# Kernel tuning notes

Hardware: AMD Instinct MI355X
Metric: run time of the kernel (lower is better)

The kernel has to match this reference:

```python
import jax, jax.numpy as jnp
import numpy as np

N, E, G, NH, H = 50000, 400000, 1024, 64, 1
EPS = 1e-5

def _bn(x):
    # BatchNorm1d in training mode, affine at init (gamma=1, beta=0), biased var
    m = x.mean(0)
    v = ((x - m) ** 2).mean(0)
    return (x - m) * jax.lax.rsqrt(v + EPS)

def _seg_softmax(logits, seg, num_segments):
    # numerically stable per-segment softmax (torch_geometric.utils.softmax)
    mx = jax.ops.segment_max(logits, seg, num_segments=num_segments)
    e = jnp.exp(logits - mx[seg])
    s = jax.ops.segment_sum(e, seg, num_segments=num_segments)
    return e / s[seg]

def setup_inputs() -> dict:
    key = jax.random.key(0)
    ks = jax.random.split(key, 16)
    p = lambda k, shape, s=0.1: jax.random.normal(k, shape, jnp.float32) * s
    return {
        "x": jax.random.normal(ks[0], (N, 92), jnp.float32),
        "edge_index": jax.random.randint(ks[1], (2, E), 0, N),
        "edge_attr": jax.random.normal(ks[2], (E, 41), jnp.float32),
        "batch": jnp.sort(jax.random.randint(ks[3], (N,), 0, G)),
        "global_feat": jax.random.normal(ks[4], (G, 103), jnp.float32),
        "emb_n_W": p(ks[5], (92, NH)), "emb_n_b": jnp.zeros((NH,), jnp.float32),
        "emb_e_W": p(ks[6], (41, NH)), "emb_e_b": jnp.zeros((NH,), jnp.float32),
        "conv_W": p(ks[7], (3, 2 * NH, H * NH)),
        "conv_att": p(ks[8], (3, H, 2 * NH)),
        "conv_bias": jnp.zeros((3, H * NH), jnp.float32),
        "comp_node_W": p(ks[9], (NH + 103, 32)), "comp_node_b": jnp.zeros((32,), jnp.float32),
        "comp_att_W": p(ks[10], (32, 1)), "comp_att_b": jnp.zeros((1,), jnp.float32),
        "fc_W": p(ks[11], (NH, 1)), "fc_b": jnp.zeros((1,), jnp.float32),
    }

def reference(x, edge_index, edge_attr, batch, global_feat,
              emb_n_W, emb_n_b, emb_e_W, emb_e_b,
              conv_W, conv_att, conv_bias,
              comp_node_W, comp_node_b, comp_att_W, comp_att_b,
              fc_W, fc_b):
    sp = jax.nn.softplus
    src, dst = edge_index[0], edge_index[1]  # PyG: x_j = x[src], aggregate by dst
    h = x @ emb_n_W + emb_n_b                              # [N, NH]
    ea = jax.nn.leaky_relu(edge_attr @ emb_e_W + emb_e_b, 0.2)  # [E, NH]
    for l in range(3):  # AGATConv layers
        hi = jnp.concatenate([h[dst], ea], -1)             # [E, 2*NH]
        hj = jnp.concatenate([h[src], ea], -1)
        ti = sp(hi @ conv_W[l]).reshape(E, H, NH)
        tj = sp(hj @ conv_W[l]).reshape(E, H, NH)
        alpha = sp(jnp.sum(jnp.concatenate([ti, tj], -1) * conv_att[l][None], -1))  # [E, H]
        alpha = sp(_bn(alpha))
        alpha = _seg_softmax(alpha, dst, N)                # segment softmax per dst node
        agg = jax.ops.segment_sum(tj * alpha[..., None], dst, num_segments=N)  # [N, H, NH]
        h = agg.reshape(N, H * NH) + conv_bias[l]
        h = sp(_bn(h))                                     # outer BatchNorm1d + softplus
    # composition attention: repeat_interleave(global_feat, counts) == gather by graph id
    gf = global_feat[batch]                                # [N, 103]
    a = sp(jnp.concatenate([h, gf], -1) @ comp_node_W + comp_node_b) @ comp_att_W + comp_att_b
    w = _seg_softmax(a, batch, G)                          # [N, 1]
    pooled = jax.ops.segment_sum(h * w, batch, num_segments=G)  # global_add_pool
    return pooled @ fc_W + fc_b                            # [G, 1]
```

## Files before the change

### kernel.cpp

```cpp
#include <hip/hip_runtime.h>
#include <hip/hip_bf16.h>
#include <hip/hip_fp16.h>
#include <math.h>


typedef unsigned short ushortt;
typedef _Float16 half2v __attribute__((ext_vector_type(2)));
typedef _Float16 f16x8 __attribute__((ext_vector_type(8)));
typedef float f32x4 __attribute__((ext_vector_type(4)));

__device__ __forceinline__ float sp_f(float x) {
  return x > 20.0f ? x : __logf(1.0f + __expf(x));
}
__device__ __forceinline__ float h2f(ushortt u) {
  union { ushortt u; __half h; } c; c.u = u;
  return __half2float(c.h);
}
__device__ __forceinline__ ushortt f2h(float f) {
  union { __half h; ushortt u; } c; c.h = __float2half(f);
  return c.u;
}
__device__ __forceinline__ float4 h4_to_f4(ushort4 u) {
  return make_float4(h2f(u.x), h2f(u.y), h2f(u.z), h2f(u.w));
}
__device__ __forceinline__ unsigned pack2h(float a, float b) {
  union { _Float16 h[2]; unsigned u; } c;
  c.h[0] = (_Float16)a; c.h[1] = (_Float16)b;
  return c.u;
}

#define SLOTS 2304

template<int K, int ACT, int BIAS, int GATHER, int FUSE_BN,
         typename IT, typename OT>
__global__ __launch_bounds__(256) void k_gemm_rt(
    const IT* __restrict__ in, const float* __restrict__ W,
    const float* __restrict__ b, OT* __restrict__ out, int R,
    const int* __restrict__ rows, const float* __restrict__ csbn, float invN)
{
  constexpr int KP = (K + 3) / 4 * 4;
  constexpr int LS = KP + 4;
  __shared__ __align__(16) float ins[64 * LS];
  __shared__ __align__(16) float Ws[KP * 64];
  __shared__ float bnm[64], bns[64];

  const int tx = threadIdx.x;
  const int b0 = blockIdx.x * 64;

  if (FUSE_BN) {
    if (tx < 64) {
      float mn = 0.f, sq = 0.f;
      #pragma unroll
      for (int bk = 0; bk < 16; ++bk) {
        mn += csbn[bk * 128 + tx];
        sq += csbn[bk * 128 + 64 + tx];
      }
      mn *= invN; sq *= invN;
      bnm[tx] = mn;
      bns[tx] = rsqrtf(sq - mn * mn + 1e-5f);
    }
    __syncthreads();
  }

  for (int i = tx; i < KP * 64; i += 256) {
    const int k = i >> 6;
    Ws[i] = (k < K) ? W[i] : 0.0f;
  }
  for (int i = tx; i < 64 * (KP / 4); i += 256) {
    const int row = i / (KP / 4);
    const int k4 = i % (KP / 4);
    long r = b0 + row; if (r >= R) r = R - 1;
    if (GATHER) r = rows[r];
    float4 v;
    if (K % 4 == 0) {
      v = *(const float4*)&((const float*)in)[r * (long)K + k4 * 4];
    } else {
      float t[4];
      #pragma unroll
      for (int j = 0; j < 4; ++j) {
        const int k = k4 * 4 + j;
        t[j] = (k < K) ? ((const float*)in)[r * (long)K + k] : 0.0f;
      }
      v = make_float4(t[0], t[1], t[2], t[3]);
    }
    if (FUSE_BN) {
      float* vv = (float*)&v;
      #pragma unroll
      for (int j = 0; j < 4; ++j) {
        const int c = k4 * 4 + j;
        vv[j] = sp_f((vv[j] - bnm[c]) * bns[c]);
      }
    }
    *(float4*)&ins[row * LS + k4 * 4] = v;
  }
  __syncthreads();

  const int lr0 = ((tx >> 6) << 4) + (((tx >> 4) & 3) << 2);
  const int c0 = (tx & 15) << 2;
  float acc[4][4];
  #pragma unroll
  for (int i = 0; i < 4; ++i)
    #pragma unroll
    for (int j = 0; j < 4; ++j) acc[i][j] = 0.0f;

  #pragma unroll 4
  for (int k4 = 0; k4 < KP / 4; ++k4) {
    float4 w[4], a[4];
    #pragma unroll
    for (int kk = 0; kk < 4; ++kk)
      w[kk] = *(const float4*)&Ws[(k4 * 4 + kk) * 64 + c0];
    #pragma unroll
    for (int ri = 0; ri < 4; ++ri)
      a[ri] = *(const float4*)&ins[(lr0 + ri) * LS + k4 * 4];
    #pragma unroll
    for (int ri = 0; ri < 4; ++ri) {
      const float* av = (const float*)&a[ri];
      #pragma unroll
      for (int kk = 0; kk < 4; ++kk) {
        acc[ri][0] = fmaf(av[kk], w[kk].x, acc[ri][0]);
        acc[ri][1] = fmaf(av[kk], w[kk].y, acc[ri][1]);
        acc[ri][2] = fmaf(av[kk], w[kk].z, acc[ri][2]);
        acc[ri][3] = fmaf(av[kk], w[kk].w, acc[ri][3]);
      }
    }
  }

  float4 bias = make_float4(0.f, 0.f, 0.f, 0.f);
  if (BIAS) bias = *(const float4*)&b[c0];
  #pragma unroll
  for (int ri = 0; ri < 4; ++ri) {
    const long r = b0 + lr0 + ri;
    if (r >= R) continue;
    float4 v;
    v.x = acc[ri][0] + bias.x; v.y = acc[ri][1] + bias.y;
    v.z = acc[ri][2] + bias.z; v.w = acc[ri][3] + bias.w;
    if (ACT == 1) {
      v.x = v.x >= 0.f ? v.x : 0.2f * v.x;  v.y = v.y >= 0.f ? v.y : 0.2f * v.y;
      v.z = v.z >= 0.f ? v.z : 0.2f * v.z;  v.w = v.w >= 0.f ? v.w : 0.2f * v.w;
    }
    if (sizeof(OT) == 4) {
      *(float4*)&out[r * 64 + c0] = v;
    } else {
      ushort4 u;
      u.x = f2h(v.x); u.y = f2h(v.y); u.z = f2h(v.z); u.w = f2h(v.w);
      *(ushort4*)&out[r * 64 + c0] = u;
    }
  }
}

__global__ __launch_bounds__(512) void k_packW(
    const float* __restrict__ convW, uint4* __restrict__ WBg)
{
  const int l3 = blockIdx.x;
  const float* W = convW + (size_t)l3 * 128 * 64 + 64 * 64;
  const int idx = threadIdx.x;
  const int kstep = idx >> 8;
  const int rem = idx & 255;
  const int ncol = rem >> 6;
  const int l = rem & 63;
  const int kbase = kstep * 32 + (l >> 4) * 8;
  const int n = ncol * 16 + (l & 15);
  ushortt tmp[8];
  #pragma unroll
  for (int j = 0; j < 8; ++j) tmp[j] = f2h(W[(kbase + j) * 64 + n]);
  WBg[l3 * 512 + idx] = *(uint4*)tmp;
}

__global__ __launch_bounds__(256) void k_efused(
    const ushortt* __restrict__ ea, const uint4* __restrict__ WBg,
    ushortt* __restrict__ out, int E, const ushortt* __restrict__ P,
    const int* __restrict__ srcp, const int* __restrict__ dstp,
    const float* __restrict__ catt, float* __restrict__ a1,
    float* __restrict__ stats)
{
  __shared__ __align__(16) unsigned char smem[17408];
  __shared__ float atts[128];
  __shared__ float ssum[4], ssq[4];
  ushortt* As   = (ushortt*)smem;
  uint4*   WB   = (uint4*)(smem + 9216);
  float*   accs = (float*)smem;

  const int tx = threadIdx.x;
  const int b0 = blockIdx.x * 64;
  const int lane = tx & 63;
  const int w = tx >> 6;

  if (tx < 128) atts[tx] = catt[tx];
  #pragma unroll
  for (int i = tx; i < 64 * 8; i += 256) {
    const int row = i >> 3;
    const int k8 = i & 7;
    long r = b0 + row; if (r >= E) r = E - 1;
    *(uint4*)&As[row * 72 + k8 * 8] = *(const uint4*)&ea[r * (long)64 + k8 * 8];
  }
  #pragma unroll
  for (int i = tx; i < 512; i += 256) WB[i] = WBg[i];
  __syncthreads();

  const int lr0 = ((tx >> 6) << 4) + (((tx >> 4) & 3) << 2);
  const int c0 = (tx & 15) << 2;
  ushort4 pdv[4], psv[4];
  #pragma unroll
  for (int ri = 0; ri < 4; ++ri) {
    long e = b0 + lr0 + ri; if (e >= E) e = E - 1;
    const int s = srcp[e];
    const int d = dstp[e];
    psv[ri] = *(const ushort4*)&P[(long)s * 64 + c0];
    pdv[ri] = *(const ushort4*)&P[(long)d * 64 + c0];
  }

  f32x4 acc0 = {0.f,0.f,0.f,0.f}, acc1 = {0.f,0.f,0.f,0.f};
  f32x4 acc2 = {0.f,0.f,0.f,0.f}, acc3 = {0.f,0.f,0.f,0.f};
  const int arow = 16 * w + (lane & 15);
  #pragma unroll
  for (int kstep = 0; kstep < 2; ++kstep) {
    const f16x8 a = __builtin_bit_cast(f16x8,
        *(const uint4*)&As[arow * 72 + kstep * 32 + (lane >> 4) * 8]);
    const int bb = kstep * 256 + lane;
    const f16x8 b0v = __builtin_bit_cast(f16x8, WB[bb]);
    const f16x8 b1v = __builtin_bit_cast(f16x8, WB[bb + 64]);
    const f16x8 b2v = __builtin_bit_cast(f16x8, WB[bb + 128]);
    const f16x8 b3v = __builtin_bit_cast(f16x8, WB[bb + 192]);
    acc0 = __builtin_amdgcn_mfma_f32_16x16x32_f16(a, b0v, acc0, 0, 0, 0);
    acc1 = __builtin_amdgcn_mfma_f32_16x16x32_f16(a, b1v, acc1, 0, 0, 0);
    acc2 = __builtin_amdgcn_mfma_f32_16x16x32_f16(a, b2v, acc2, 0, 0, 0);
    acc3 = __builtin_amdgcn_mfma_f32_16x16x32_f16(a, b3v, acc3, 0, 0, 0);
  }
  __syncthreads();

  {
    const int rbase = 16 * w + (lane >> 4) * 4;
    const int cb = lane & 15;
    #pragma unroll
    for (int reg = 0; reg < 4; ++reg) {
      accs[(rbase + reg) * 68 + cb]      = acc0[reg];
      accs[(rbase + reg) * 68 + 16 + cb] = acc1[reg];
      accs[(rbase + reg) * 68 + 32 + cb] = acc2[reg];
      accs[(rbase + reg) * 68 + 48 + cb] = acc3[reg];
    }
  }
  __syncthreads();

  float s1 = 0.f, s2 = 0.f;
  #pragma unroll
  for (int ri = 0; ri < 4; ++ri) {
    const long e = b0 + lr0 + ri;
    float part = 0.0f;
    if (e < E) {
      const float4 Pd = h4_to_f4(pdv[ri]);
      const float4 Ps = h4_to_f4(psv[ri]);
      const float4 m = *(const float4*)&accs[(lr0 + ri) * 68 + c0];
      float tj[4];
      const float ti0 = sp_f(Pd.x + m.x);
      const float ti1 = sp_f(Pd.y + m.y);
      const float ti2 = sp_f(Pd.z + m.z);
      const float ti3 = sp_f(Pd.w + m.w);
      tj[0] = sp_f(Ps.x + m.x);
      tj[1] = sp_f(Ps.y + m.y);
      tj[2] = sp_f(Ps.z + m.z);
      tj[3] = sp_f(Ps.w + m.w);
      ushort4 u;
      u.x = f2h(tj[0]); u.y = f2h(tj[1]); u.z = f2h(tj[2]); u.w = f2h(tj[3]);
      *(ushort4*)&out[e * 64 + c0] = u;
      part = ti0 * atts[c0] + ti1 * atts[c0 + 1] + ti2 * atts[c0 + 2] + ti3 * atts[c0 + 3]
           + tj[0] * atts[64 + c0] + tj[1] * atts[64 + c0 + 1]
           + tj[2] * atts[64 + c0 + 2] + tj[3] * atts[64 + c0 + 3];
    }
    #pragma unroll
    for (int off = 8; off; off >>= 1) part += __shfl_xor(part, off);
    if ((tx & 15) == 0 && e < E) {
      const float v = sp_f(part);
      a1[e] = v;
      s1 += v; s2 += v * v;
    }
  }
  s1 += __shfl_xor(s1, 16); s2 += __shfl_xor(s2, 16);
  s1 += __shfl_xor(s1, 32); s2 += __shfl_xor(s2, 32);
  if ((tx & 63) == 0) { ssum[tx >> 6] = s1; ssq[tx >> 6] = s2; }
  __syncthreads();
  if (tx == 0) {
    const int bk = blockIdx.x & 63;
    atomicAdd(&stats[bk], ssum[0] + ssum[1] + ssum[2] + ssum[3]);
    atomicAdd(&stats[64 + bk], ssq[0] + ssq[1] + ssq[2] + ssq[3]);
  }
}

__global__ __launch_bounds__(256) void k_count(
    const int* __restrict__ dst, int* __restrict__ counts, int E)
{
  for (int i = blockIdx.x * 256 + threadIdx.x; i < E; i += gridDim.x * 256)
    atomicAdd(&counts[dst[i]], 1);
}

__global__ __launch_bounds__(256) void k_scan1(
    const int* __restrict__ counts, int* __restrict__ offs,
    int* __restrict__ bsum, int N)
{
  __shared__ int sm[256];
  const int t = threadIdx.x;
  const int idx = blockIdx.x * 256 + t;
  const int v = (idx < N) ? counts[idx] : 0;
  sm[t] = v;
  __syncthreads();
  for (int off = 1; off < 256; off <<= 1) {
    const int u = (t >= off) ? sm[t - off] : 0;
    __syncthreads();
    sm[t] += u;
    __syncthreads();
  }
  if (idx < N) offs[idx] = sm[t] - v;
  if (t == 255) bsum[blockIdx.x] = sm[255];
}

__global__ __launch_bounds__(1024) void k_scan2(int* __restrict__ bsum, int SB)
{
  __shared__ int sm[1024];
  const int t = threadIdx.x;
  const int v = (t < SB) ? bsum[t] : 0;
  sm[t] = v;
  __syncthreads();
  for (int off = 1; off < 1024; off <<= 1) {
    const int u = (t >= off) ? sm[t - off] : 0;
    __syncthreads();
    sm[t] += u;
    __syncthreads();
  }
  if (t < SB) bsum[t] = sm[t] - v;
}

__global__ __launch_bounds__(256) void k_scan3(
    int* __restrict__ offs, const int* __restrict__ bsum, int N, int E)
{
  const int idx = blockIdx.x * 256 + threadIdx.x;
  if (idx < N) offs[idx] += bsum[blockIdx.x];
  if (idx == 0) offs[N] = E;
}

__global__ __launch_bounds__(256) void k_fill(
    const int* __restrict__ dst, const int* __restrict__ offs,
    int* __restrict__ cursors, int* __restrict__ eids, int E)
{
  for (int i = blockIdx.x * 256 + threadIdx.x; i < E; i += gridDim.x * 256) {
    const int d = dst[i];
    eids[offs[d] + atomicAdd(&cursors[d], 1)] = i;
  }
}

__global__ __launch_bounds__(256) void k_permidx(
    const int* __restrict__ eids, const int* __restrict__ eidx,
    int* __restrict__ srcp, int* __restrict__ dstp, int E)
{
  for (int i = blockIdx.x * 256 + threadIdx.x; i < E; i += gridDim.x * 256) {
    const int e = eids[i];
    srcp[i] = eidx[e];
    dstp[i] = eidx[(long)E + e];
  }
}

__global__ __launch_bounds__(256) void k_aggregate(
    const int* __restrict__ offs, const float* __restrict__ a1p,
    const ushortt* __restrict__ Mp, const float* __restrict__ stats,
    float invE, float* __restrict__ aggn, float* __restrict__ cs, int N)
{
  __shared__ float sm_mean, sm_scl;
  const int tx = threadIdx.x;
  if (tx < 64) {
    float s1 = stats[tx];
    float s2 = stats[64 + tx];
    #pragma unroll
    for (int off = 32; off; off >>= 1) {
      s1 += __shfl_xor(s1, off);
      s2 += __shfl_xor(s2, off);
    }
    if (tx == 0) {
      const float mean = s1 * invE;
      sm_mean = mean;
      sm_scl = rsqrtf(s2 * invE - mean * mean + 1e-5f);
    }
  }
  __syncthreads();
  const float mean = sm_mean;
  const float scl = sm_scl;

  const int t = tx & 63;
  const int wid = tx >> 6;
  float s = 0.f, s2 = 0.f;
  const long step = (long)gridDim.x * 4;
  for (long n = (long)blockIdx.x * 4 + wid; n < N; n += step) {
    const int o0 = offs[n];
    const int o1 = offs[n + 1];
    float av = 0.f, sew = 0.f;
    #pragma unroll 4
    for (int i = o0; i < o1; ++i) {
      const float w = __expf(sp_f((a1p[i] - mean) * scl));
      av = fmaf(h2f(Mp[(long)i * 64 + t]), w, av);
      sew += w;
    }
    const float v = (o1 > o0) ? av / sew : 0.0f;
    aggn[n * 64 + t] = v;
    s += v; s2 += v * v;
  }
  __shared__ float b1[256], b2[256];
  b1[tx] = s; b2[tx] = s2;
  __syncthreads();
  if (tx < 64) {
    const int bank = (blockIdx.x & 15) * 128;
    atomicAdd(&cs[bank + t], b1[t] + b1[64 + t] + b1[128 + t] + b1[192 + t]);
    atomicAdd(&cs[bank + 64 + t], b2[t] + b2[64 + t] + b2[128 + t] + b2[192 + t]);
  }
}

__global__ __launch_bounds__(256) void k_hnew(
    const float* __restrict__ aggn, const float* __restrict__ cs,
    float invN, float* __restrict__ h, int N)
{
  const int c = threadIdx.x & 63;
  const int r = threadIdx.x >> 6;
  float mn = 0.f, sq = 0.f;
  #pragma unroll
  for (int bk = 0; bk < 16; ++bk) {
    mn += cs[bk * 128 + c];
    sq += cs[bk * 128 + 64 + c];
  }
  mn *= invN; sq *= invN;
  const float scl = rsqrtf(sq - mn * mn + 1e-5f);
  for (long n = (long)blockIdx.x * 4 + r; n < N; n += (long)gridDim.x * 4)
    h[n * 64 + c] = sp_f((aggn[n * 64 + c] - mn) * scl);
}

#define QSS 170
__global__ __launch_bounds__(256) void k_comp(
    const float* __restrict__ h, const float* __restrict__ gf,
    const int* __restrict__ batch, const float* __restrict__ Wc,
    const float* __restrict__ bc, const float* __restrict__ aw,
    const float* __restrict__ ab, float* __restrict__ aN, int N)
{
  __shared__ __align__(16) float qs[64 * QSS];
  __shared__ __align__(16) float Wcs[167 * 32];
  __shared__ float aws[32], bcs[32];
  const int tx = threadIdx.x;
  const int b0 = blockIdx.x * 64;
  for (int i = tx; i < 167 * 32; i += 256) Wcs[i] = Wc[i];
  if (tx < 32) { aws[tx] = aw[tx]; bcs[tx] = bc[tx]; }
  for (int i = tx; i < 64 * 16; i += 256) {
    const int n = i >> 4;
    const int c4 = (i & 15) << 2;
    long r = b0 + n; if (r >= N) r = N - 1;
    *(float4*)&qs[n * QSS + c4] = *(const float4*)&h[r * 64 + c4];
  }
  for (int i = tx; i < 64 * 103; i += 256) {
    const int n = i / 103;
    const int c = i % 103;
    long r = b0 + n; if (r >= N) r = N - 1;
    qs[n * QSS + 64 + c] = gf[(long)batch[r] * 103 + c];
  }
  __syncthreads();

  const int n = tx >> 2;
  const int colg = (tx & 3) << 3;
  float acc[8];
  #pragma unroll
  for (int j = 0; j < 8; ++j) acc[j] = 0.f;
  #pragma unroll 2
  for (int k = 0; k < 167; ++k) {
    const float q = qs[n * QSS + k];
    const float4 w0 = *(const float4*)&Wcs[k * 32 + colg];
    const float4 w1 = *(const float4*)&Wcs[k * 32 + colg + 4];
    acc[0] = fmaf(q, w0.x, acc[0]);
    acc[1] = fmaf(q, w0.y, acc[1]);
    acc[2] = fmaf(q, w0.z, acc[2]);
    acc[3] = fmaf(q, w0.w, acc[3]);
    acc[4] = fmaf(q, w1.x, acc[4]);
    acc[5] = fmaf(q, w1.y, acc[5]);
    acc[6] = fmaf(q, w1.z, acc[6]);
    acc[7] = fmaf(q, w1.w, acc[7]);
  }
  float val = 0.f;
  #pragma unroll
  for (int j = 0; j < 8; ++j)
    val += sp_f(acc[j] + bcs[colg + j]) * aws[colg + j];
  val += __shfl_xor(val, 1);
  val += __shfl_xor(val, 2);
  const long r = b0 + n;
  if ((tx & 3) == 0 && r < N) aN[r] = val + ab[0];
}

__global__ __launch_bounds__(64) void k_pool(
    const float* __restrict__ h, const float* __restrict__ aN,
    const int* __restrict__ batch, const float* __restrict__ fcW,
    const float* __restrict__ fcb, float* __restrict__ out, int N, int G)
{
  const int g = blockIdx.x;
  const int t = threadIdx.x;
  int lo = 0, hi = N;
  while (lo < hi) { int mid = (lo + hi) >> 1; if (batch[mid] < g) lo = mid + 1; else hi = mid; }
  const int s = lo;
  hi = N;
  while (lo < hi) { int mid = (lo + hi) >> 1; if (batch[mid] < g + 1) lo = mid + 1; else hi = mid; }
  const int e2 = lo;
  if (s >= e2) { if (t == 0) out[g] = fcb[0]; return; }
  float mx = -1e30f;
  for (int i = s + t; i < e2; i += 64) mx = fmaxf(mx, aN[i]);
  #pragma unroll
  for (int off = 32; off; off >>= 1) mx = fmaxf(mx, __shfl_xor(mx, off));
  float se = 0.f;
  for (int i = s + t; i < e2; i += 64) se += __expf(aN[i] - mx);
  #pragma unroll
  for (int off = 32; off; off >>= 1) se += __shfl_xor(se, off);
  float acc = 0.f;
  for (int n = s; n < e2; ++n) {
    const float w = __expf(aN[n] - mx);
    acc = fmaf(h[(long)n * 64 + t], w, acc);
  }
  float part = (acc / se) * fcW[t];
  #pragma unroll
  for (int off = 32; off; off >>= 1) part += __shfl_xor(part, off);
  if (t == 0) out[g] = part + fcb[0];
}

extern "C" void kernel_launch(void* const* d_in, const int* in_sizes, int n_in,
                              void* d_out, int out_size, void* d_ws, size_t ws_size,
                              hipStream_t stream)
{
  const float* x     = (const float*)d_in[0];
  const int*   eidx  = (const int*)  d_in[1];
  const float* eattr = (const float*)d_in[2];
  const int*   batch = (const int*)  d_in[3];
  const float* gfeat = (const float*)d_in[4];
  const float* embnW = (const float*)d_in[5];
  const float* embnb = (const float*)d_in[6];
  const float* embeW = (const float*)d_in[7];
  const float* embeb = (const float*)d_in[8];
  const float* convW = (const float*)d_in[9];
  const float* convA = (const float*)d_in[10];
  const float* compW = (const float*)d_in[12];
  const float* compb = (const float*)d_in[13];
  const float* attW  = (const float*)d_in[14];
  const float* attb  = (const float*)d_in[15];
  const float* fcW   = (const float*)d_in[16];
  const float* fcb   = (const float*)d_in[17];
  float* out = (float*)d_out;

  const int N = in_sizes[0] / 92;
  const int E = in_sizes[1] / 2;
  const int G = in_sizes[4] / 103;
  const float invN = 1.0f / (float)N;
  const float invE = 1.0f / (float)E;

  char* pw = (char*)d_ws;
  float* h     = (float*)pw;  pw += (size_t)N * 64 * 4;
  float* aggn  = (float*)pw;  pw += (size_t)N * 64 * 4;
  float* aE    = (float*)pw;  pw += (size_t)E * 4;
  float* statsB = (float*)pw; pw += 3 * SLOTS * 4;
  float* aN    = (float*)pw;  pw += (size_t)N * 4;
  int* counts  = (int*)pw;    pw += (size_t)N * 4;
  int* cursors = (int*)pw;    pw += (size_t)N * 4;
  int* offs    = (int*)pw;    pw += ((size_t)N + 1) * 4;
  int* bsum    = (int*)pw;    pw += 1024 * 4;
  int* eids    = (int*)pw;    pw += (size_t)E * 4;
  int* srcp    = (int*)pw;    pw += (size_t)E * 4;
  int* dstp    = (int*)pw;    pw += (size_t)E * 4;
  pw = (char*)(((size_t)pw + 63) & ~(size_t)63);
  uint4* WBg   = (uint4*)pw;   pw += 3 * 512 * 16;
  ushortt* Pp  = (ushortt*)pw; pw += (size_t)N * 64 * 2;
  ushortt* ea  = (ushortt*)pw; pw += (size_t)E * 64 * 2;
  ushortt* M   = (ushortt*)pw;

  const int gE64 = (E + 63) / 64;
  const int gN64 = (N + 63) / 64;
  const int SB = (N + 255) / 256;

  hipMemsetAsync(counts, 0, 2 * (size_t)N * sizeof(int), stream);
  hipMemsetAsync(statsB, 0, 3 * SLOTS * sizeof(float), stream);
  k_count<<<2048, 256, 0, stream>>>(eidx + E, counts, E);
  k_scan1<<<SB, 256, 0, stream>>>(counts, offs, bsum, N);
  k_scan2<<<1, 1024, 0, stream>>>(bsum, SB);
  k_scan3<<<SB, 256, 0, stream>>>(offs, bsum, N, E);
  k_fill<<<2048, 256, 0, stream>>>(eidx + E, offs, cursors, eids, E);
  k_permidx<<<2048, 256, 0, stream>>>(eids, eidx, srcp, dstp, E);
  k_packW<<<3, 512, 0, stream>>>(convW, WBg);

  k_gemm_rt<92, 0, 1, 0, 0, float, float><<<gN64, 256, 0, stream>>>(
      x, embnW, embnb, h, N, nullptr, nullptr, 0.f);
  k_gemm_rt<41, 1, 1, 1, 0, float, ushortt><<<gE64, 256, 0, stream>>>(
      eattr, embeW, embeb, ea, E, eids, nullptr, 0.f);

  for (int l = 0; l < 3; ++l) {
    const float* Wl = convW + (size_t)l * 128 * 64;
    const float* Al = convA + (size_t)l * 128;
    float* statsL = statsB + (size_t)l * SLOTS;
    if (l == 0) {
      k_gemm_rt<64, 0, 0, 0, 0, float, ushortt><<<gN64, 256, 0, stream>>>(
          h, Wl, nullptr, Pp, N, nullptr, nullptr, 0.f);
    } else {
      k_gemm_rt<64, 0, 0, 0, 1, float, ushortt><<<gN64, 256, 0, stream>>>(
          aggn, Wl, nullptr, Pp, N, nullptr,
          statsB + (size_t)(l - 1) * SLOTS + 128, invN);
    }
    k_efused<<<gE64, 256, 0, stream>>>(ea, WBg + (size_t)l * 512, M, E,
                                       Pp, srcp, dstp, Al, aE, statsL);
    k_aggregate<<<2048, 256, 0, stream>>>(offs, aE, M, statsL,
                                          invE, aggn, statsL + 128, N);
  }

  k_hnew<<<2048, 256, 0, stream>>>(aggn, statsB + 2 * SLOTS + 128, invN, h, N);
  k_comp<<<gN64, 256, 0, stream>>>(h, gfeat, batch, compW, compb, attW, attb, aN, N);
  k_pool<<<G, 64, 0, stream>>>(h, aN, batch, fcW, fcb, out, N, G);

  (void)n_in; (void)out_size; (void)ws_size;
}
```

Before: 475.6 us.

## Embed edges in original order then permute fp16 rows; fuse index permutation into fill

The edge-embedding GEMM no longer gathers its 41-float input rows by sorted edge id. It writes fp16 output in original order to a temp buffer, and a new kernel permutes the 128-byte rows into dst-sorted order. The fill kernel now writes srcp/dstp directly, which removes the separate permidx pass. The shared-memory row stride is also padded to avoid bank conflicts. The cost is an extra E×128B buffer plus a read/write pass in exchange for coalesced GEMM input loads.

```diff
diff --git a/kernel.cpp b/kernel.cpp
--- a/kernel.cpp
+++ b/kernel.cpp
@@ -5,7 +5,6 @@
 
 
 typedef unsigned short ushortt;
-typedef _Float16 half2v __attribute__((ext_vector_type(2)));
 typedef _Float16 f16x8 __attribute__((ext_vector_type(8)));
 typedef float f32x4 __attribute__((ext_vector_type(4)));
 
@@ -23,23 +22,18 @@
 __device__ __forceinline__ float4 h4_to_f4(ushort4 u) {
   return make_float4(h2f(u.x), h2f(u.y), h2f(u.z), h2f(u.w));
 }
-__device__ __forceinline__ unsigned pack2h(float a, float b) {
-  union { _Float16 h[2]; unsigned u; } c;
-  c.h[0] = (_Float16)a; c.h[1] = (_Float16)b;
-  return c.u;
-}
 
 #define SLOTS 2304
 
-template<int K, int ACT, int BIAS, int GATHER, int FUSE_BN,
-         typename IT, typename OT>
+template<int K, int ACT, int BIAS, int FUSE_BN, typename IT, typename OT>
 __global__ __launch_bounds__(256) void k_gemm_rt(
     const IT* __restrict__ in, const float* __restrict__ W,
     const float* __restrict__ b, OT* __restrict__ out, int R,
-    const int* __restrict__ rows, const float* __restrict__ csbn, float invN)
+    const float* __restrict__ csbn, float invN)
 {
   constexpr int KP = (K + 3) / 4 * 4;
-  constexpr int LS = KP + 4;
+  constexpr int LS0 = KP + 4;
+  constexpr int LS = ((4 * LS0) % 32 == 0) ? LS0 + 4 : LS0;
   __shared__ __align__(16) float ins[64 * LS];
   __shared__ __align__(16) float Ws[KP * 64];
   __shared__ float bnm[64], bns[64];
@@ -70,7 +64,6 @@
     const int row = i / (KP / 4);
     const int k4 = i % (KP / 4);
     long r = b0 + row; if (r >= R) r = R - 1;
-    if (GATHER) r = rows[r];
     float4 v;
     if (K % 4 == 0) {
       v = *(const float4*)&((const float*)in)[r * (long)K + k4 * 4];
@@ -145,6 +138,19 @@
       u.x = f2h(v.x); u.y = f2h(v.y); u.z = f2h(v.z); u.w = f2h(v.w);
       *(ushort4*)&out[r * 64 + c0] = u;
     }
+  }
+}
+
+__global__ __launch_bounds__(256) void k_permE(
+    const unsigned* __restrict__ ea_tmp, const int* __restrict__ eids,
+    unsigned* __restrict__ ea, int E)
+{
+  const long total = (long)E * 32;
+  for (long idx = (long)blockIdx.x * 256 + threadIdx.x; idx < total;
+       idx += (long)gridDim.x * 256) {
+    const long i = idx >> 5;
+    const int wd = (int)(idx & 31);
+    ea[i * 32 + wd] = ea_tmp[(long)eids[i] * 32 + wd];
   }
 }
 
@@ -337,23 +343,17 @@
 }
 
 __global__ __launch_bounds__(256) void k_fill(
-    const int* __restrict__ dst, const int* __restrict__ offs,
-    int* __restrict__ cursors, int* __restrict__ eids, int E)
+    const int* __restrict__ src, const int* __restrict__ dst,
+    const int* __restrict__ offs, int* __restrict__ cursors,
+    int* __restrict__ eids, int* __restrict__ srcp, int* __restrict__ dstp,
+    int E)
 {
   for (int i = blockIdx.x * 256 + threadIdx.x; i < E; i += gridDim.x * 256) {
     const int d = dst[i];
-    eids[offs[d] + atomicAdd(&cursors[d], 1)] = i;
-  }
-}
-
-__global__ __launch_bounds__(256) void k_permidx(
-    const int* __restrict__ eids, const int* __restrict__ eidx,
-    int* __restrict__ srcp, int* __restrict__ dstp, int E)
-{
-  for (int i = blockIdx.x * 256 + threadIdx.x; i < E; i += gridDim.x * 256) {
-    const int e = eids[i];
-    srcp[i] = eidx[e];
-    dstp[i] = eidx[(long)E + e];
+    const int pos = offs[d] + atomicAdd(&cursors[d], 1);
+    eids[pos] = i;
+    srcp[pos] = src[i];
+    dstp[pos] = d;
   }
 }
 
@@ -564,7 +564,8 @@
   uint4* WBg   = (uint4*)pw;   pw += 3 * 512 * 16;
   ushortt* Pp  = (ushortt*)pw; pw += (size_t)N * 64 * 2;
   ushortt* ea  = (ushortt*)pw; pw += (size_t)E * 64 * 2;
-  ushortt* M   = (ushortt*)pw;
+  ushortt* M   = (ushortt*)pw; pw += (size_t)E * 64 * 2;
+  ushortt* eaT = (ushortt*)pw;
 
   const int gE64 = (E + 63) / 64;
   const int gN64 = (N + 63) / 64;
@@ -576,25 +577,27 @@
   k_scan1<<<SB, 256, 0, stream>>>(counts, offs, bsum, N);
   k_scan2<<<1, 1024, 0, stream>>>(bsum, SB);
   k_scan3<<<SB, 256, 0, stream>>>(offs, bsum, N, E);
-  k_fill<<<2048, 256, 0, stream>>>(eidx + E, offs, cursors, eids, E);
-  k_permidx<<<2048, 256, 0, stream>>>(eids, eidx, srcp, dstp, E);
+  k_fill<<<2048, 256, 0, stream>>>(eidx, eidx + E, offs, cursors,
+                                   eids, srcp, dstp, E);
   k_packW<<<3, 512, 0, stream>>>(convW, WBg);
 
-  k_gemm_rt<92, 0, 1, 0, 0, float, float><<<gN64, 256, 0, stream>>>(
-      x, embnW, embnb, h, N, nullptr, nullptr, 0.f);
-  k_gemm_rt<41, 1, 1, 1, 0, float, ushortt><<<gE64, 256, 0, stream>>>(
-      eattr, embeW, embeb, ea, E, eids, nullptr, 0.f);
+  k_gemm_rt<92, 0, 1, 0, float, float><<<gN64, 256, 0, stream>>>(
+      x, embnW, embnb, h, N, nullptr, 0.f);
+  k_gemm_rt<41, 1, 1, 0, float, ushortt><<<gE64, 256, 0, stream>>>(
+      eattr, embeW, embeb, eaT, E, nullptr, 0.f);
+  k_permE<<<4096, 256, 0, stream>>>((const unsigned*)eaT, eids,
+                                    (unsigned*)ea, E);
 
   for (int l = 0; l < 3; ++l) {
     const float* Wl = convW + (size_t)l * 128 * 64;
     const float* Al = convA + (size_t)l * 128;
     float* statsL = statsB + (size_t)l * SLOTS;
     if (l == 0) {
-      k_gemm_rt<64, 0, 0, 0, 0, float, ushortt><<<gN64, 256, 0, stream>>>(
-          h, Wl, nullptr, Pp, N, nullptr, nullptr, 0.f);
+      k_gemm_rt<64, 0, 0, 0, float, ushortt><<<gN64, 256, 0, stream>>>(
+          h, Wl, nullptr, Pp, N, nullptr, 0.f);
     } else {
-      k_gemm_rt<64, 0, 0, 0, 1, float, ushortt><<<gN64, 256, 0, stream>>>(
-          aggn, Wl, nullptr, Pp, N, nullptr,
+      k_gemm_rt<64, 0, 0, 1, float, ushortt><<<gN64, 256, 0, stream>>>(
+          aggn, Wl, nullptr, Pp, N,
           statsB + (size_t)(l - 1) * SLOTS + 128, invN);
     }
     k_efused<<<gE64, 256, 0, stream>>>(ea, WBg + (size_t)l * 512, M, E,
```

Result: slower. 523.9 us (+10.2%).
